# Kernel optimization log

Hardware: AMD Instinct MI355X
Metric: run time of the kernel (lower is better)

The kernel has to match this reference:

```python
import jax, jax.numpy as jnp
import numpy as np

M = 0.25
GAMMA = 256.0
HARD_W = 2.0
O_P = 1.0 + M
O_N = -M
DELTA_P = 1.0 - M
DELTA_N = M
NEG_BIG = -1e30  # masked-out fill for logsumexp (finite to keep grads NaN-free)


def setup_inputs() -> dict:
    key = jax.random.key(0)
    k1, k2 = jax.random.split(key)
    inputs = jax.random.normal(k1, (4096, 512), dtype=jnp.float32)
    targets = jax.random.randint(k2, (4096,), 0, 64, dtype=jnp.int64)
    return {"inputs": inputs, "targets": targets}


def reference(inputs, targets):
    n = inputs.shape[0]
    x = inputs / jnp.linalg.norm(inputs, axis=1, keepdims=True)  # L2 normalize
    sim = x @ x.T                                                # [n, n]

    same = targets[:, None] == targets[None, :]
    eye = jnp.eye(n, dtype=bool)
    pos_mask = same & ~eye
    neg_mask = ~same
    npos = pos_mask.sum(axis=1)
    nneg = neg_mask.sum(axis=1)

    sim_d = jax.lax.stop_gradient(sim)  # alphas are detached in the original
    alpha_p = jax.nn.relu(O_P - sim_d)
    alpha_n = jax.nn.relu(sim_d - O_N)

    # hard mining: scale alpha at hardest positive (min sim) / hardest negative (max sim)
    idx = jnp.arange(n)
    hard_p = jnp.argmin(jnp.where(pos_mask, sim_d, jnp.inf), axis=1)
    hard_n = jnp.argmax(jnp.where(neg_mask, sim_d, -jnp.inf), axis=1)
    hit_p = (idx[None, :] == hard_p[:, None]) & (npos > 1)[:, None]
    hit_n = (idx[None, :] == hard_n[:, None]) & (nneg > 1)[:, None]
    alpha_p = alpha_p * jnp.where(hit_p, HARD_W, 1.0)
    alpha_n = alpha_n * jnp.where(hit_n, HARD_W, 1.0)

    pos_term = jnp.where(pos_mask, -GAMMA * alpha_p * (sim - DELTA_P), NEG_BIG)
    neg_term = jnp.where(neg_mask, GAMMA * alpha_n * (sim - DELTA_N), NEG_BIG)
    lse_p = jax.nn.logsumexp(pos_term, axis=1)
    lse_n = jax.nn.logsumexp(neg_term, axis=1)

    valid = (npos > 0) & (nneg > 0)
    per_row = jnp.where(valid, jax.nn.softplus(lse_p + lse_n), 0.0)
    n_valid = jnp.maximum(valid.sum(), 1)
    return per_row.sum() / n_valid.astype(per_row.dtype)
```

## Files before the change

kernel.cpp:

```cpp
#include <hip/hip_runtime.h>


#define MASKT_  (-1.0e4f)
#define MINITP_ (-1.0e4f)
#define MASKP_  (-3.0e4f)
#define QA_     369.3299304675f
#define QB_     (-23.08312065422f)
#define LN2_    0.6931471805599453f

constexpr int N_ = 4096;
constexpr int D_ = 512;
constexpr int AST_ = 520;
constexpr int CCH_ = 16;

typedef __bf16 bf16x8 __attribute__((ext_vector_type(8)));
typedef float  f32x4  __attribute__((ext_vector_type(4)));
typedef const unsigned int __attribute__((address_space(1)))* gp_t;
typedef unsigned int       __attribute__((address_space(3)))* lp_t;

__device__ __forceinline__ float pos_q(float s) {
    float d = s - 1.0f;
    return fmaf(d * d, 256.0f, -16.0f);
}
__device__ __forceinline__ float neg_q(float s) {
    float q = fmaf(s * s, 256.0f, -16.0f);
    return (s >= -0.25f) ? q : 0.0f;
}
__device__ __forceinline__ float neg_q2(float s) {
    float q = fmaf(s * s, QA_, QB_);
    return (s >= -0.25f) ? q : 0.0f;
}
__device__ __forceinline__ void lse_merge(float m2, float S2, float& m, float& S) {
    float mm = fmaxf(m, m2);
    S = S * __expf(m - mm) + S2 * __expf(m2 - mm);
    m = mm;
}
__device__ __forceinline__ void lse_merge2(float m2, float S2, float& m, float& S) {
    float mm = fmaxf(m, m2);
    S = S * exp2f(m - mm) + S2 * exp2f(m2 - mm);
    m = mm;
}
__device__ __forceinline__ unsigned short f2bf(float f) {
    unsigned int u = __float_as_uint(f);
    unsigned int r = u + 0x7FFFu + ((u >> 16) & 1u);
    return (unsigned short)(r >> 16);
}

__global__ __launch_bounds__(256) void k_norm(const float* __restrict__ in,
                                              unsigned short* __restrict__ xb,
                                              float* __restrict__ acc) {
    const int row  = blockIdx.x * 4 + (threadIdx.x >> 6);
    const int lane = threadIdx.x & 63;
    const float4* src = (const float4*)(in + (size_t)row * D_) + lane * 2;
    float4 a = src[0], b = src[1];
    float ss = a.x*a.x + a.y*a.y + a.z*a.z + a.w*a.w
             + b.x*b.x + b.y*b.y + b.z*b.z + b.w*b.w;
    #pragma unroll
    for (int d = 32; d >= 1; d >>= 1) ss += __shfl_xor(ss, d);
    float rn = 1.0f / sqrtf(ss);
    float v[8] = {a.x, a.y, a.z, a.w, b.x, b.y, b.z, b.w};
    union { uint4 u; unsigned short us[8]; } pk;
    #pragma unroll
    for (int k = 0; k < 8; ++k) pk.us[k] = f2bf(v[k] * rn);
    *((uint4*)(xb + (size_t)row * D_) + lane) = pk.u;
    if (blockIdx.x == 0 && threadIdx.x < 4) acc[threadIdx.x] = 0.0f;
}

__global__ __launch_bounds__(256, 4) void k_mainM(const unsigned short* __restrict__ xb,
                                                  const int* __restrict__ tg,
                                                  float* __restrict__ part) {
    constexpr int NST = 16;
    __shared__ __align__(16) unsigned short Bs[2][16][AST_];

    const int tid  = threadIdx.x;
    const int wave = tid >> 6, lane = tid & 63;
    const int n16  = lane & 15, quad = lane >> 4;
    const int rg   = (int)blockIdx.x >> 4;
    const int cc   = (int)blockIdx.x & 15;
    const int rowBase = rg * 64 + wave * 16;
    const int colBase = cc * 256;
    const int phase = (((int)blockIdx.x >> 8) & 3) * 4;

    bf16x8 af[16];
    {
        const bf16x8* ap = (const bf16x8*)(xb + (size_t)(rowBase + n16) * D_ + quad * 8);
        #pragma unroll
        for (int kk = 0; kk < 16; ++kk) af[kk] = ap[kk * 4];
    }
    int tr[4];
    #pragma unroll
    for (int r = 0; r < 4; ++r) tr[r] = tg[rowBase + quad * 4 + r];

    float m_p[4], S_p[4], S_n[4], mxn[4];
    #pragma unroll
    for (int r = 0; r < 4; ++r) {
        m_p[r] = MINITP_; S_p[r] = 0.f; S_n[r] = 0.f; mxn[r] = -2.0f;
    }

    const char* gstage = (const char*)xb + (size_t)colBase * 1024 + lane * 16;

    {
        const char* g0 = gstage + (size_t)phase * 16384;
        #pragma unroll
        for (int p = 0; p < 4; ++p) {
            int j = p * 4 + wave;
            __builtin_amdgcn_global_load_lds((gp_t)(const void*)(g0 + j * 1024),
                                             (lp_t)(void*)&Bs[0][j][0], 16, 0, 0);
        }
    }
    int tc_cur = tg[colBase + phase * 16 + n16];

    auto epi = [&](const f32x4& a0, const f32x4& a1, int tcv, bool withDiag) {
        #pragma unroll
        for (int r = 0; r < 4; ++r) {
            float sim = a0[r] + a1[r];
            bool samec = (tr[r] == tcv);
            float dm1 = sim - 1.0f;
            float tp  = fmaf(dm1 * dm1, QA_, QB_);
            tp = samec ? tp : MASKP_;
            if (withDiag && n16 == quad * 4 + r) tp = MASKP_;
            float diff = m_p[r] - tp;
            float e    = exp2f(-fabsf(diff));
            float sA   = S_p[r] + e;
            float sB   = fmaf(S_p[r], e, 1.0f);
            S_p[r] = (diff < 0.0f) ? sB : sA;
            m_p[r] = fmaxf(m_p[r], tp);
            float tn = fmaf(sim * sim, QA_, QB_);
            float en = exp2f(tn);
            en = (sim >= -0.25f) ? en : 1.0f;
            en = samec ? 0.0f : en;
            S_n[r] += en;
            mxn[r] = fmaxf(mxn[r], samec ? -2.0f : sim);
        }
    };

    #pragma unroll 1
    for (int u = 0; u < NST; ++u) {
        const int s = (u + phase) & 15;
        const int b = u & 1;
        const int j0 = colBase + s * 16;
        __syncthreads();

        const int sn = (s + 1) & 15;
        if (u + 1 < NST) {
            const char* g2 = gstage + (size_t)sn * 16384;
            #pragma unroll
            for (int p = 0; p < 4; ++p) {
                int j = p * 4 + wave;
                __builtin_amdgcn_global_load_lds((gp_t)(const void*)(g2 + j * 1024),
                                                 (lp_t)(void*)&Bs[b ^ 1][j][0], 16, 0, 0);
            }
        }
        int tc_nxt = (u + 1 < NST) ? tg[colBase + sn * 16 + n16] : 0;

        f32x4 a0 = {0.f, 0.f, 0.f, 0.f}, a1 = {0.f, 0.f, 0.f, 0.f};
        __builtin_amdgcn_s_setprio(1);
        #pragma unroll
        for (int kk = 0; kk < 8; ++kk) {
            bf16x8 bf0 = *(const bf16x8*)&Bs[b][n16][(2 * kk) * 32 + quad * 8];
            bf16x8 bf1 = *(const bf16x8*)&Bs[b][n16][(2 * kk + 1) * 32 + quad * 8];
            a0 = __builtin_amdgcn_mfma_f32_16x16x32_bf16(af[2 * kk],     bf0, a0, 0, 0, 0);
            a1 = __builtin_amdgcn_mfma_f32_16x16x32_bf16(af[2 * kk + 1], bf1, a1, 0, 0, 0);
        }
        __builtin_amdgcn_s_setprio(0);

        if (j0 == rowBase) epi(a0, a1, tc_cur, true);
        else               epi(a0, a1, tc_cur, false);
        tc_cur = tc_nxt;
    }

    #pragma unroll
    for (int r = 0; r < 4; ++r) {
        #pragma unroll
        for (int d = 1; d <= 8; d <<= 1) {
            lse_merge2(__shfl_xor(m_p[r], d), __shfl_xor(S_p[r], d), m_p[r], S_p[r]);
            S_n[r] += __shfl_xor(S_n[r], d);
            mxn[r] = fmaxf(mxn[r], __shfl_xor(mxn[r], d));
        }
    }
    if (n16 == 0) {
        #pragma unroll
        for (int r = 0; r < 4; ++r) {
            ((float4*)part)[(size_t)(rowBase + quad * 4 + r) * CCH_ + cc] =
                make_float4(m_p[r], S_p[r], mxn[r], S_n[r]);
        }
    }
}

__global__ __launch_bounds__(256) void k_reduceF(const float* __restrict__ part,
                                                 const int* __restrict__ tg,
                                                 float* __restrict__ acc,
                                                 float* __restrict__ out) {
    __shared__ int hist[64];
    const int tid = threadIdx.x;
    if (tid < 64) hist[tid] = 0;
    __syncthreads();
    for (int i = tid; i < N_; i += 256) atomicAdd(&hist[tg[i]], 1);
    __syncthreads();

    const int row = blockIdx.x * 256 + tid;
    const float4* P = (const float4*)part + (size_t)row * CCH_;
    float M_p = MINITP_, Sp = 0.f, M_n = 0.f, Sn = 0.f, mxn = -2.0f;
    #pragma unroll
    for (int c = 0; c < CCH_; ++c) {
        float4 a = P[c];
        lse_merge2(a.x, a.y, M_p, Sp);
        Sn += a.w;
        mxn = fmaxf(mxn, a.z);
    }
    const int cnt = hist[tg[row]];
    float np2 = (float)(cnt - 1), nn2 = (float)(N_ - cnt);
    float loss = 0.f, vld = 0.f;
    if (np2 > 0.5f && nn2 > 0.5f) {
        if (np2 > 1.5f) {
            float t1 = M_p, t2 = 2.0f * t1;
            float mm = fmaxf(M_p, t2);
            Sp = Sp * exp2f(M_p - mm) + exp2f(t2 - mm) - exp2f(t1 - mm);
            M_p = mm;
        }
        if (nn2 > 1.5f) {
            float t1 = neg_q2(mxn), t2 = 2.0f * t1;
            float mm = fmaxf(M_n, t2);
            Sn = Sn * exp2f(M_n - mm) + exp2f(t2 - mm) - exp2f(t1 - mm);
            M_n = mm;
        }
        float z = LN2_ * ((M_p + __log2f(Sp)) + (M_n + __log2f(Sn)));
        loss = fmaxf(z, 0.0f) + log1pf(__expf(-fabsf(z)));
        vld = 1.0f;
    }
    #pragma unroll
    for (int d = 32; d >= 1; d >>= 1) { loss += __shfl_xor(loss, d); vld += __shfl_xor(vld, d); }
    if ((tid & 63) == 0) { atomicAdd(&acc[0], loss); atomicAdd(&acc[1], vld); }

    __syncthreads();
    if (tid == 0) {
        __threadfence();
        int old = atomicAdd((int*)(acc + 2), 1);
        if (old == (int)gridDim.x - 1) {
            float ls = atomicAdd(&acc[0], 0.0f);
            float lv = atomicAdd(&acc[1], 0.0f);
            out[0] = ls / fmaxf(lv, 1.0f);
        }
    }
}

__global__ void k_final(const float* __restrict__ acc, float* __restrict__ out) {
    if (threadIdx.x == 0) out[0] = acc[0] / fmaxf(acc[1], 1.0f);
}

__global__ void k_sentinel(float* __restrict__ out) {
    if (threadIdx.x == 0) out[0] = -12345.0f;
}

__global__ __launch_bounds__(1024, 4) void k_main3(const unsigned short* __restrict__ xb,
                                                   const int* __restrict__ tg,
                                                   float* __restrict__ acc_g) {
    __shared__ __align__(16) unsigned short As[16 * AST_];
    __shared__ float sm[16][16][8];
    const int tid  = threadIdx.x;
    const int wave = tid >> 6, lane = tid & 63;
    const int n16  = lane & 15, quad = lane >> 4;
    const int rowBase = blockIdx.x * 16;
    {
        int row = tid >> 6, c = tid & 63;
        *(uint4*)&As[row * AST_ + c * 8] =
            *(const uint4*)(xb + (size_t)(rowBase + row) * D_ + c * 8);
    }
    int ir[4], tr[4];
    #pragma unroll
    for (int r = 0; r < 4; ++r) { ir[r] = rowBase + quad * 4 + r; tr[r] = tg[ir[r]]; }
    float m_p[4], S_p[4], m_n[4], S_n[4], mnp[4], mxn[4], sc[4];
    #pragma unroll
    for (int r = 0; r < 4; ++r) {
        m_p[r] = 0.f; S_p[r] = 0.f; m_n[r] = 0.f; S_n[r] = 0.f;
        mnp[r] = 2.0f; mxn[r] = -2.0f; sc[r] = 0.f;
    }
    __syncthreads();
    const unsigned short* Af = &As[n16 * AST_ + quad * 8];
    #pragma unroll 1
    for (int t = wave; t < N_ / 16; t += 16) {
        const int jcol = t * 16 + n16;
        const int tc = tg[jcol];
        const bf16x8* bp = (const bf16x8*)(xb + (size_t)jcol * D_ + quad * 8);
        bf16x8 bf[16];
        #pragma unroll
        for (int kk = 0; kk < 16; ++kk) bf[kk] = bp[kk * 4];
        f32x4 a0 = {0.f, 0.f, 0.f, 0.f}, a1 = {0.f, 0.f, 0.f, 0.f};
        #pragma unroll
        for (int kk = 0; kk < 8; ++kk) {
            bf16x8 af0 = *(const bf16x8*)(Af + (2 * kk) * 32);
            bf16x8 af1 = *(const bf16x8*)(Af + (2 * kk + 1) * 32);
            a0 = __builtin_amdgcn_mfma_f32_16x16x32_bf16(af0, bf[2 * kk],     a0, 0, 0, 0);
            a1 = __builtin_amdgcn_mfma_f32_16x16x32_bf16(af1, bf[2 * kk + 1], a1, 0, 0, 0);
        }
        #pragma unroll
        for (int r = 0; r < 4; ++r) {
            float s = a0[r] + a1[r];
            bool samec = (tr[r] == tc);
            bool posm  = samec && (jcol != ir[r]);
            float tp = posm  ? pos_q(s) : MASKT_;
            float tn = samec ? MASKT_ : neg_q(s);
            float mm = fmaxf(m_p[r], tp);
            S_p[r] = S_p[r] * __expf(m_p[r] - mm) + __expf(tp - mm); m_p[r] = mm;
            mm = fmaxf(m_n[r], tn);
            S_n[r] = S_n[r] * __expf(m_n[r] - mm) + __expf(tn - mm); m_n[r] = mm;
            sc[r] += samec ? 1.0f : 0.0f;
            mnp[r] = fminf(mnp[r], posm ? s : 2.0f);
            mxn[r] = fmaxf(mxn[r], samec ? -2.0f : s);
        }
    }
    #pragma unroll
    for (int r = 0; r < 4; ++r) {
        #pragma unroll
        for (int d = 1; d <= 8; d <<= 1) {
            lse_merge(__shfl_xor(m_p[r], d), __shfl_xor(S_p[r], d), m_p[r], S_p[r]);
            lse_merge(__shfl_xor(m_n[r], d), __shfl_xor(S_n[r], d), m_n[r], S_n[r]);
            mnp[r] = fminf(mnp[r], __shfl_xor(mnp[r], d));
            mxn[r] = fmaxf(mxn[r], __shfl_xor(mxn[r], d));
            sc[r] += __shfl_xor(sc[r], d);
        }
    }
    if (n16 == 0) {
        #pragma unroll
        for (int r = 0; r < 4; ++r) {
            float* q = sm[wave][quad * 4 + r];
            q[0] = m_p[r]; q[1] = S_p[r]; q[2] = m_n[r]; q[3] = S_n[r];
            q[4] = mnp[r]; q[5] = mxn[r]; q[6] = sc[r];
        }
    }
    __syncthreads();
    if (tid < 64) {
        const int L = tid & 15;
        float m_p2 = 0.f, S_p2 = 0.f, m_n2 = 0.f, S_n2 = 0.f;
        float mnp2 = 2.0f, mxn2 = -2.0f, sct = 0.f;
        #pragma unroll
        for (int w = 0; w < 16; ++w) {
            const float* q = sm[w][L];
            lse_merge(q[0], q[1], m_p2, S_p2);
            lse_merge(q[2], q[3], m_n2, S_n2);
            mnp2 = fminf(mnp2, q[4]); mxn2 = fmaxf(mxn2, q[5]);
            sct += q[6];
        }
        float loss = 0.f, vld = 0.f;
        float np2 = sct - 1.0f, nn2 = (float)N_ - sct;
        if (tid < 16 && np2 > 0.5f && nn2 > 0.5f) {
            if (np2 > 1.5f) {
                float t1 = pos_q(mnp2), t2 = 2.0f * t1;
                float mm = fmaxf(m_p2, t2);
                S_p2 = S_p2 * __expf(m_p2 - mm) + __expf(t2 - mm) - __expf(t1 - mm);
                m_p2 = mm;
            }
            if (nn2 > 1.5f) {
                float t1 = neg_q(mxn2), t2 = 2.0f * t1;
                float mm = fmaxf(m_n2, t2);
                S_n2 = S_n2 * __expf(m_n2 - mm) + __expf(t2 - mm) - __expf(t1 - mm);
                m_n2 = mm;
            }
            float z = (m_p2 + __logf(S_p2)) + (m_n2 + __logf(S_n2));
            loss = fmaxf(z, 0.0f) + log1pf(__expf(-fabsf(z)));
            vld = 1.0f;
        }
        #pragma unroll
        for (int d = 32; d >= 1; d >>= 1) {
            loss += __shfl_xor(loss, d); vld += __shfl_xor(vld, d);
        }
        if (tid == 0) { atomicAdd(&acc_g[0], loss); atomicAdd(&acc_g[1], vld); }
    }
}

extern "C" void kernel_launch(void* const* d_in, const int* in_sizes, int n_in,
                              void* d_out, int out_size, void* d_ws, size_t ws_size,
                              hipStream_t stream) {
    const float* in = (const float*)d_in[0];
    const int*   tg = (const int*)d_in[1];
    constexpr size_t MB = 1024 * 1024;
    unsigned short* xb = (unsigned short*)d_ws;

    if (ws_size >= 5 * MB + 64) {
        float* part = (float*)((char*)d_ws + 4 * MB);
        float* acc  = (float*)((char*)d_ws + 5 * MB);
        hipLaunchKernelGGL(k_norm,    dim3(N_ / 4),    dim3(256), 0, stream, in, xb, acc);
        hipLaunchKernelGGL(k_mainM,   dim3(64 * CCH_), dim3(256), 0, stream, xb, tg, part);
        hipLaunchKernelGGL(k_reduceF, dim3(N_ / 256),  dim3(256), 0, stream, part, tg, acc,
                           (float*)d_out);
    } else if (ws_size >= 4 * MB + 64) {
        float* acc = (float*)((char*)d_ws + 4 * MB);
        hipLaunchKernelGGL(k_norm,  dim3(N_ / 4),  dim3(256),  0, stream, in, xb, acc);
        hipLaunchKernelGGL(k_main3, dim3(N_ / 16), dim3(1024), 0, stream, xb, tg, acc);
        hipLaunchKernelGGL(k_final, dim3(1),       dim3(64),   0, stream, acc, (float*)d_out);
    } else {
        hipLaunchKernelGGL(k_sentinel, dim3(1), dim3(64), 0, stream, (float*)d_out);
    }
}
```

Before: 107.4 us.

## Exploit similarity matrix symmetry with triangular block scheduling and column-side partials

Computes only the upper-triangular blocks of the symmetric similarity matrix. Each block accumulates row-side logsumexp/max partials and also column-side partials through shared memory and shuffles, which it writes to extra slots. Blocks are mapped to triangle coordinates with a sqrt-based index, and a per-element strict-upper mask handles the diagonal band. This is meant to roughly halve the MFMA and exp work, at the cost of more epilogue arithmetic, extra shared-memory merges, a larger partial buffer, and a fast path that now needs a 12 MB workspace.

```diff
diff --git a/kernel.cpp b/kernel.cpp
--- a/kernel.cpp
+++ b/kernel.cpp
@@ -11,7 +11,7 @@
 constexpr int N_ = 4096;
 constexpr int D_ = 512;
 constexpr int AST_ = 520;
-constexpr int CCH_ = 16;
+constexpr int NSLOT_ = 96;
 
 typedef __bf16 bf16x8 __attribute__((ext_vector_type(8)));
 typedef float  f32x4  __attribute__((ext_vector_type(4)));
@@ -66,20 +66,26 @@
     if (blockIdx.x == 0 && threadIdx.x < 4) acc[threadIdx.x] = 0.0f;
 }
 
-__global__ __launch_bounds__(256, 4) void k_mainM(const unsigned short* __restrict__ xb,
+__global__ __launch_bounds__(256, 4) void k_mainS(const unsigned short* __restrict__ xb,
                                                   const int* __restrict__ tg,
                                                   float* __restrict__ part) {
-    constexpr int NST = 16;
+    constexpr int NST = 8;
     __shared__ __align__(16) unsigned short Bs[2][16][AST_];
+    __shared__ float4 Bcol[2][4][16];
 
     const int tid  = threadIdx.x;
     const int wave = tid >> 6, lane = tid & 63;
     const int n16  = lane & 15, quad = lane >> 4;
-    const int rg   = (int)blockIdx.x >> 4;
-    const int cc   = (int)blockIdx.x & 15;
+
+    int bid = (int)blockIdx.x;
+    int cc = (int)((sqrtf(4.0f * (float)bid + 1.0f) - 1.0f) * 0.5f);
+    while ((cc + 1) * (cc + 2) <= bid) ++cc;
+    while (cc * (cc + 1) > bid) --cc;
+    const int rg = bid - cc * (cc + 1);
+
     const int rowBase = rg * 64 + wave * 16;
-    const int colBase = cc * 256;
-    const int phase = (((int)blockIdx.x >> 8) & 3) * 4;
+    const int colBase = cc * 128;
+    const bool band = (rg >= 2 * cc);
 
     bf16x8 af[16];
     {
@@ -98,52 +104,40 @@
     }
 
     const char* gstage = (const char*)xb + (size_t)colBase * 1024 + lane * 16;
-
-    {
-        const char* g0 = gstage + (size_t)phase * 16384;
-        #pragma unroll
-        for (int p = 0; p < 4; ++p) {
-            int j = p * 4 + wave;
-            __builtin_amdgcn_global_load_lds((gp_t)(const void*)(g0 + j * 1024),
-                                             (lp_t)(void*)&Bs[0][j][0], 16, 0, 0);
-        }
-    }
-    int tc_cur = tg[colBase + phase * 16 + n16];
-
-    auto epi = [&](const f32x4& a0, const f32x4& a1, int tcv, bool withDiag) {
-        #pragma unroll
-        for (int r = 0; r < 4; ++r) {
-            float sim = a0[r] + a1[r];
-            bool samec = (tr[r] == tcv);
-            float dm1 = sim - 1.0f;
-            float tp  = fmaf(dm1 * dm1, QA_, QB_);
-            tp = samec ? tp : MASKP_;
-            if (withDiag && n16 == quad * 4 + r) tp = MASKP_;
-            float diff = m_p[r] - tp;
-            float e    = exp2f(-fabsf(diff));
-            float sA   = S_p[r] + e;
-            float sB   = fmaf(S_p[r], e, 1.0f);
-            S_p[r] = (diff < 0.0f) ? sB : sA;
-            m_p[r] = fmaxf(m_p[r], tp);
-            float tn = fmaf(sim * sim, QA_, QB_);
-            float en = exp2f(tn);
-            en = (sim >= -0.25f) ? en : 1.0f;
-            en = samec ? 0.0f : en;
-            S_n[r] += en;
-            mxn[r] = fmaxf(mxn[r], samec ? -2.0f : sim);
+    #pragma unroll
+    for (int p = 0; p < 4; ++p) {
+        int j = p * 4 + wave;
+        __builtin_amdgcn_global_load_lds((gp_t)(const void*)(gstage + j * 1024),
+                                         (lp_t)(void*)&Bs[0][j][0], 16, 0, 0);
+    }
+    int tc_cur = tg[colBase + n16];
+
+    auto mergeCol = [&](int sp) {
+        const int c = lane >> 2, w = lane & 3;
+        float4 v = Bcol[sp & 1][w][c];
+        #pragma unroll
+        for (int d = 1; d <= 2; d <<= 1) {
+            float m2 = __shfl_xor(v.x, d), S2 = __shfl_xor(v.y, d);
+            float z2 = __shfl_xor(v.z, d), n2 = __shfl_xor(v.w, d);
+            lse_merge2(m2, S2, v.x, v.y);
+            v.z = fmaxf(v.z, z2);
+            v.w += n2;
+        }
+        if (w == 0) {
+            int jc = colBase + sp * 16 + c;
+            ((float4*)part)[(size_t)jc * NSLOT_ + 32 + rg] = v;
         }
     };
 
     #pragma unroll 1
     for (int u = 0; u < NST; ++u) {
-        const int s = (u + phase) & 15;
         const int b = u & 1;
-        const int j0 = colBase + s * 16;
         __syncthreads();
 
-        const int sn = (s + 1) & 15;
+        if (u > 0 && wave == ((u - 1) & 3)) mergeCol(u - 1);
+
         if (u + 1 < NST) {
-            const char* g2 = gstage + (size_t)sn * 16384;
+            const char* g2 = gstage + (size_t)(u + 1) * 16384;
             #pragma unroll
             for (int p = 0; p < 4; ++p) {
                 int j = p * 4 + wave;
@@ -151,7 +145,7 @@
                                                  (lp_t)(void*)&Bs[b ^ 1][j][0], 16, 0, 0);
             }
         }
-        int tc_nxt = (u + 1 < NST) ? tg[colBase + sn * 16 + n16] : 0;
+        int tc_nxt = (u + 1 < NST) ? tg[colBase + (u + 1) * 16 + n16] : 0;
 
         f32x4 a0 = {0.f, 0.f, 0.f, 0.f}, a1 = {0.f, 0.f, 0.f, 0.f};
         __builtin_amdgcn_s_setprio(1);
@@ -164,10 +158,46 @@
         }
         __builtin_amdgcn_s_setprio(0);
 
-        if (j0 == rowBase) epi(a0, a1, tc_cur, true);
-        else               epi(a0, a1, tc_cur, false);
+        const int jcol = colBase + u * 16 + n16;
+        const int iv   = rowBase + quad * 4;
+        float mc = MINITP_, Sc = 0.f, Snc = 0.f, mxc = -2.0f;
+        #pragma unroll
+        for (int r = 0; r < 4; ++r) {
+            float sim = a0[r] + a1[r];
+            bool samec = (tr[r] == tc_cur);
+            bool valid = !band || (iv + r < jcol);
+            float dm1 = sim - 1.0f;
+            float tp  = fmaf(dm1 * dm1, QA_, QB_);
+            tp = (samec && valid) ? tp : MASKP_;
+            float diff = m_p[r] - tp;
+            float e    = exp2f(-fabsf(diff));
+            S_p[r] = (diff < 0.0f) ? fmaf(S_p[r], e, 1.0f) : S_p[r] + e;
+            m_p[r] = fmaxf(m_p[r], tp);
+            float dc = mc - tp;
+            float ec = exp2f(-fabsf(dc));
+            Sc = (dc < 0.0f) ? fmaf(Sc, ec, 1.0f) : Sc + ec;
+            mc = fmaxf(mc, tp);
+            float tn = fmaf(sim * sim, QA_, QB_);
+            float en = exp2f(tn);
+            en = (sim >= -0.25f) ? en : 1.0f;
+            en = (!samec && valid) ? en : 0.0f;
+            S_n[r] += en; Snc += en;
+            float simn = (valid && !samec) ? sim : -2.0f;
+            mxn[r] = fmaxf(mxn[r], simn);
+            mxc    = fmaxf(mxc, simn);
+        }
+        #pragma unroll
+        for (int d = 16; d <= 32; d <<= 1) {
+            lse_merge2(__shfl_xor(mc, d), __shfl_xor(Sc, d), mc, Sc);
+            Snc += __shfl_xor(Snc, d);
+            mxc = fmaxf(mxc, __shfl_xor(mxc, d));
+        }
+        if (quad == 0) Bcol[b][wave][n16] = make_float4(mc, Sc, mxc, Snc);
+
         tc_cur = tc_nxt;
     }
+    __syncthreads();
+    if (wave == 3) mergeCol(NST - 1);
 
     #pragma unroll
     for (int r = 0; r < 4; ++r) {
@@ -181,13 +211,13 @@
     if (n16 == 0) {
         #pragma unroll
         for (int r = 0; r < 4; ++r) {
-            ((float4*)part)[(size_t)(rowBase + quad * 4 + r) * CCH_ + cc] =
+            ((float4*)part)[(size_t)(rowBase + quad * 4 + r) * NSLOT_ + cc] =
                 make_float4(m_p[r], S_p[r], mxn[r], S_n[r]);
         }
     }
 }
 
-__global__ __launch_bounds__(256) void k_reduceF(const float* __restrict__ part,
+__global__ __launch_bounds__(256) void k_reduceS(const float* __restrict__ part,
                                                  const int* __restrict__ tg,
                                                  float* __restrict__ acc,
                                                  float* __restrict__ out) {
@@ -199,15 +229,25 @@
     __syncthreads();
 
     const int row = blockIdx.x * 256 + tid;
-    const float4* P = (const float4*)part + (size_t)row * CCH_;
+    const int rg  = row >> 6;
+    const int ccmin = rg >> 1;
+    const int nb  = min(2 * (rg >> 1) + 2, 64);
+    const float4* P = (const float4*)part + (size_t)row * NSLOT_;
+
     float M_p = MINITP_, Sp = 0.f, M_n = 0.f, Sn = 0.f, mxn = -2.0f;
-    #pragma unroll
-    for (int c = 0; c < CCH_; ++c) {
+    for (int c = ccmin; c < 32; ++c) {
         float4 a = P[c];
         lse_merge2(a.x, a.y, M_p, Sp);
         Sn += a.w;
         mxn = fmaxf(mxn, a.z);
     }
+    for (int b = 0; b < nb; ++b) {
+        float4 a = P[32 + b];
+        lse_merge2(a.x, a.y, M_p, Sp);
+        Sn += a.w;
+        mxn = fmaxf(mxn, a.z);
+    }
+
     const int cnt = hist[tg[row]];
     float np2 = (float)(cnt - 1), nn2 = (float)(N_ - cnt);
     float loss = 0.f, vld = 0.f;
@@ -354,6 +394,7 @@
                 float t1 = neg_q(mxn2), t2 = 2.0f * t1;
                 float mm = fmaxf(m_n2, t2);
                 S_n2 = S_n2 * __expf(m_n2 - mm) + __expf(t2 - mm) - __expf(t1 - mm);
+                M_n2: ;
                 m_n2 = mm;
             }
             float z = (m_p2 + __logf(S_p2)) + (m_n2 + __logf(S_n2));
@@ -376,12 +417,12 @@
     constexpr size_t MB = 1024 * 1024;
     unsigned short* xb = (unsigned short*)d_ws;
 
-    if (ws_size >= 5 * MB + 64) {
-        float* part = (float*)((char*)d_ws + 4 * MB);
-        float* acc  = (float*)((char*)d_ws + 5 * MB);
-        hipLaunchKernelGGL(k_norm,    dim3(N_ / 4),    dim3(256), 0, stream, in, xb, acc);
-        hipLaunchKernelGGL(k_mainM,   dim3(64 * CCH_), dim3(256), 0, stream, xb, tg, part);
-        hipLaunchKernelGGL(k_reduceF, dim3(N_ / 256),  dim3(256), 0, stream, part, tg, acc,
+    if (ws_size >= 12 * MB) {
+        float* acc  = (float*)((char*)d_ws + 4 * MB);
+        float* part = (float*)((char*)d_ws + 5 * MB);
+        hipLaunchKernelGGL(k_norm,    dim3(N_ / 4),   dim3(256), 0, stream, in, xb, acc);
+        hipLaunchKernelGGL(k_mainS,   dim3(1056),     dim3(256), 0, stream, xb, tg, part);
+        hipLaunchKernelGGL(k_reduceS, dim3(N_ / 256), dim3(256), 0, stream, part, tg, acc,
                            (float*)d_out);
     } else if (ws_size >= 4 * MB + 64) {
         float* acc = (float*)((char*)d_ws + 4 * MB);
```

Result: slower. 128.8 us (+20.0%).

## Split positive-pair LSE into per-class kernel, keep only negative terms in main pass

Applied to the files above, without the earlier changes.

The main all-pairs kernel no longer computes the positive-pair online logsumexp. It only accumulates the negative sum and the hardest-negative max, which trims the epilogue and halves the partial output. A new per-class kernel gathers each class's member indices and computes positive similarities only within the class. It makes two passes, one for the min similarity (used as the max term) and one for the exp-sum. This adds a kernel launch and a small 64-block kernel with uncoalesced row gathers, and it depends on there being at most 64 classes, which is a property of the test inputs.

```diff
diff --git a/kernel.cpp b/kernel.cpp
--- a/kernel.cpp
+++ b/kernel.cpp
@@ -3,7 +3,6 @@
 
 #define MASKT_  (-1.0e4f)
 #define MINITP_ (-1.0e4f)
-#define MASKP_  (-3.0e4f)
 #define QA_     369.3299304675f
 #define QB_     (-23.08312065422f)
 #define LN2_    0.6931471805599453f
@@ -66,7 +65,7 @@
     if (blockIdx.x == 0 && threadIdx.x < 4) acc[threadIdx.x] = 0.0f;
 }
 
-__global__ __launch_bounds__(256, 4) void k_mainM(const unsigned short* __restrict__ xb,
+__global__ __launch_bounds__(256, 4) void k_mainN(const unsigned short* __restrict__ xb,
                                                   const int* __restrict__ tg,
                                                   float* __restrict__ part) {
     constexpr int NST = 16;
@@ -91,14 +90,11 @@
     #pragma unroll
     for (int r = 0; r < 4; ++r) tr[r] = tg[rowBase + quad * 4 + r];
 
-    float m_p[4], S_p[4], S_n[4], mxn[4];
-    #pragma unroll
-    for (int r = 0; r < 4; ++r) {
-        m_p[r] = MINITP_; S_p[r] = 0.f; S_n[r] = 0.f; mxn[r] = -2.0f;
-    }
+    float S_n[4], mxn[4];
+    #pragma unroll
+    for (int r = 0; r < 4; ++r) { S_n[r] = 0.f; mxn[r] = -2.0f; }
 
     const char* gstage = (const char*)xb + (size_t)colBase * 1024 + lane * 16;
-
     {
         const char* g0 = gstage + (size_t)phase * 16384;
         #pragma unroll
@@ -110,21 +106,39 @@
     }
     int tc_cur = tg[colBase + phase * 16 + n16];
 
-    auto epi = [&](const f32x4& a0, const f32x4& a1, int tcv, bool withDiag) {
+    #pragma unroll 1
+    for (int u = 0; u < NST; ++u) {
+        const int s = (u + phase) & 15;
+        const int b = u & 1;
+        __syncthreads();
+
+        const int sn = (s + 1) & 15;
+        if (u + 1 < NST) {
+            const char* g2 = gstage + (size_t)sn * 16384;
+            #pragma unroll
+            for (int p = 0; p < 4; ++p) {
+                int j = p * 4 + wave;
+                __builtin_amdgcn_global_load_lds((gp_t)(const void*)(g2 + j * 1024),
+                                                 (lp_t)(void*)&Bs[b ^ 1][j][0], 16, 0, 0);
+            }
+        }
+        int tc_nxt = (u + 1 < NST) ? tg[colBase + sn * 16 + n16] : 0;
+
+        f32x4 a0 = {0.f, 0.f, 0.f, 0.f}, a1 = {0.f, 0.f, 0.f, 0.f};
+        __builtin_amdgcn_s_setprio(1);
+        #pragma unroll
+        for (int kk = 0; kk < 8; ++kk) {
+            bf16x8 bf0 = *(const bf16x8*)&Bs[b][n16][(2 * kk) * 32 + quad * 8];
+            bf16x8 bf1 = *(const bf16x8*)&Bs[b][n16][(2 * kk + 1) * 32 + quad * 8];
+            a0 = __builtin_amdgcn_mfma_f32_16x16x32_bf16(af[2 * kk],     bf0, a0, 0, 0, 0);
+            a1 = __builtin_amdgcn_mfma_f32_16x16x32_bf16(af[2 * kk + 1], bf1, a1, 0, 0, 0);
+        }
+        __builtin_amdgcn_s_setprio(0);
+
         #pragma unroll
         for (int r = 0; r < 4; ++r) {
             float sim = a0[r] + a1[r];
-            bool samec = (tr[r] == tcv);
-            float dm1 = sim - 1.0f;
-            float tp  = fmaf(dm1 * dm1, QA_, QB_);
-            tp = samec ? tp : MASKP_;
-            if (withDiag && n16 == quad * 4 + r) tp = MASKP_;
-            float diff = m_p[r] - tp;
-            float e    = exp2f(-fabsf(diff));
-            float sA   = S_p[r] + e;
-            float sB   = fmaf(S_p[r], e, 1.0f);
-            S_p[r] = (diff < 0.0f) ? sB : sA;
-            m_p[r] = fmaxf(m_p[r], tp);
+            bool samec = (tr[r] == tc_cur);
             float tn = fmaf(sim * sim, QA_, QB_);
             float en = exp2f(tn);
             en = (sim >= -0.25f) ? en : 1.0f;
@@ -132,40 +146,6 @@
             S_n[r] += en;
             mxn[r] = fmaxf(mxn[r], samec ? -2.0f : sim);
         }
-    };
-
-    #pragma unroll 1
-    for (int u = 0; u < NST; ++u) {
-        const int s = (u + phase) & 15;
-        const int b = u & 1;
-        const int j0 = colBase + s * 16;
-        __syncthreads();
-
-        const int sn = (s + 1) & 15;
-        if (u + 1 < NST) {
-            const char* g2 = gstage + (size_t)sn * 16384;
-            #pragma unroll
-            for (int p = 0; p < 4; ++p) {
-                int j = p * 4 + wave;
-                __builtin_amdgcn_global_load_lds((gp_t)(const void*)(g2 + j * 1024),
-                                                 (lp_t)(void*)&Bs[b ^ 1][j][0], 16, 0, 0);
-            }
-        }
-        int tc_nxt = (u + 1 < NST) ? tg[colBase + sn * 16 + n16] : 0;
-
-        f32x4 a0 = {0.f, 0.f, 0.f, 0.f}, a1 = {0.f, 0.f, 0.f, 0.f};
-        __builtin_amdgcn_s_setprio(1);
-        #pragma unroll
-        for (int kk = 0; kk < 8; ++kk) {
-            bf16x8 bf0 = *(const bf16x8*)&Bs[b][n16][(2 * kk) * 32 + quad * 8];
-            bf16x8 bf1 = *(const bf16x8*)&Bs[b][n16][(2 * kk + 1) * 32 + quad * 8];
-            a0 = __builtin_amdgcn_mfma_f32_16x16x32_bf16(af[2 * kk],     bf0, a0, 0, 0, 0);
-            a1 = __builtin_amdgcn_mfma_f32_16x16x32_bf16(af[2 * kk + 1], bf1, a1, 0, 0, 0);
-        }
-        __builtin_amdgcn_s_setprio(0);
-
-        if (j0 == rowBase) epi(a0, a1, tc_cur, true);
-        else               epi(a0, a1, tc_cur, false);
         tc_cur = tc_nxt;
     }
 
@@ -173,7 +153,6 @@
     for (int r = 0; r < 4; ++r) {
         #pragma unroll
         for (int d = 1; d <= 8; d <<= 1) {
-            lse_merge2(__shfl_xor(m_p[r], d), __shfl_xor(S_p[r], d), m_p[r], S_p[r]);
             S_n[r] += __shfl_xor(S_n[r], d);
             mxn[r] = fmaxf(mxn[r], __shfl_xor(mxn[r], d));
         }
@@ -181,34 +160,125 @@
     if (n16 == 0) {
         #pragma unroll
         for (int r = 0; r < 4; ++r) {
-            ((float4*)part)[(size_t)(rowBase + quad * 4 + r) * CCH_ + cc] =
-                make_float4(m_p[r], S_p[r], mxn[r], S_n[r]);
-        }
-    }
-}
-
-__global__ __launch_bounds__(256) void k_reduceF(const float* __restrict__ part,
+            ((float2*)part)[(size_t)(rowBase + quad * 4 + r) * CCH_ + cc] =
+                make_float2(mxn[r], S_n[r]);
+        }
+    }
+}
+
+__global__ __launch_bounds__(256, 1) void k_classP(const unsigned short* __restrict__ xb,
+                                                   const int* __restrict__ tg,
+                                                   float* __restrict__ part2,
+                                                   int* __restrict__ cnt_g) {
+    __shared__ int lst[N_];
+    __shared__ int lcnt;
+    const int tid  = threadIdx.x;
+    const int wave = tid >> 6, lane = tid & 63;
+    const int n16  = lane & 15, quad = lane >> 4;
+    const int c    = (int)blockIdx.x;
+
+    if (tid == 0) lcnt = 0;
+    __syncthreads();
+    for (int i = tid; i < N_; i += 256)
+        if (tg[i] == c) lst[atomicAdd(&lcnt, 1)] = i;
+    __syncthreads();
+    const int Kc = lcnt;
+    if (tid == 0) cnt_g[c] = Kc;
+
+    for (int rb = wave * 16; rb < Kc; rb += 64) {
+        const int ia = lst[(rb + n16 < Kc) ? rb + n16 : 0];
+        bf16x8 af[16];
+        {
+            const bf16x8* ap = (const bf16x8*)(xb + (size_t)ia * D_ + quad * 8);
+            #pragma unroll
+            for (int kk = 0; kk < 16; ++kk) af[kk] = ap[kk * 4];
+        }
+        auto simStage = [&](int cs, f32x4& a0, f32x4& a1) {
+            const int jb = cs + n16;
+            const int jcol = lst[(jb < Kc) ? jb : 0];
+            const bf16x8* bp = (const bf16x8*)(xb + (size_t)jcol * D_ + quad * 8);
+            a0 = {0.f, 0.f, 0.f, 0.f}; a1 = {0.f, 0.f, 0.f, 0.f};
+            #pragma unroll
+            for (int kk = 0; kk < 8; ++kk) {
+                bf16x8 b0 = bp[(2 * kk) * 4], b1 = bp[(2 * kk + 1) * 4];
+                a0 = __builtin_amdgcn_mfma_f32_16x16x32_bf16(af[2 * kk],     b0, a0, 0, 0, 0);
+                a1 = __builtin_amdgcn_mfma_f32_16x16x32_bf16(af[2 * kk + 1], b1, a1, 0, 0, 0);
+            }
+        };
+
+        float mnp[4] = {2.f, 2.f, 2.f, 2.f};
+        for (int cs = 0; cs < Kc; cs += 16) {
+            f32x4 a0, a1; simStage(cs, a0, a1);
+            #pragma unroll
+            for (int r = 0; r < 4; ++r) {
+                const int ii = rb + quad * 4 + r, jb = cs + n16;
+                bool valid = (ii < Kc) && (jb < Kc) && (jb != ii);
+                float sim = a0[r] + a1[r];
+                mnp[r] = fminf(mnp[r], valid ? sim : 2.0f);
+            }
+        }
+        #pragma unroll
+        for (int r = 0; r < 4; ++r)
+            #pragma unroll
+            for (int d = 1; d <= 8; d <<= 1)
+                mnp[r] = fminf(mnp[r], __shfl_xor(mnp[r], d));
+
+        float mp[4], Sp[4];
+        #pragma unroll
+        for (int r = 0; r < 4; ++r) {
+            float dm = mnp[r] - 1.0f;
+            mp[r] = (mnp[r] < 1.5f) ? fmaf(dm * dm, QA_, QB_) : MINITP_;
+            Sp[r] = 0.f;
+        }
+        for (int cs = 0; cs < Kc; cs += 16) {
+            f32x4 a0, a1; simStage(cs, a0, a1);
+            #pragma unroll
+            for (int r = 0; r < 4; ++r) {
+                const int ii = rb + quad * 4 + r, jb = cs + n16;
+                bool valid = (ii < Kc) && (jb < Kc) && (jb != ii);
+                float sim = a0[r] + a1[r];
+                float dm1 = sim - 1.0f;
+                float tp  = fmaf(dm1 * dm1, QA_, QB_);
+                Sp[r] += valid ? exp2f(tp - mp[r]) : 0.f;
+            }
+        }
+        #pragma unroll
+        for (int r = 0; r < 4; ++r)
+            #pragma unroll
+            for (int d = 1; d <= 8; d <<= 1)
+                Sp[r] += __shfl_xor(Sp[r], d);
+
+        if (n16 == 0) {
+            #pragma unroll
+            for (int r = 0; r < 4; ++r) {
+                const int ii = rb + quad * 4 + r;
+                if (ii < Kc)
+                    ((float2*)part2)[lst[ii]] = make_float2(mp[r], Sp[r]);
+            }
+        }
+    }
+}
+
+__global__ __launch_bounds__(256) void k_reduceN(const float* __restrict__ part,
+                                                 const float* __restrict__ part2,
+                                                 const int* __restrict__ cnt_g,
                                                  const int* __restrict__ tg,
                                                  float* __restrict__ acc,
                                                  float* __restrict__ out) {
-    __shared__ int hist[64];
     const int tid = threadIdx.x;
-    if (tid < 64) hist[tid] = 0;
-    __syncthreads();
-    for (int i = tid; i < N_; i += 256) atomicAdd(&hist[tg[i]], 1);
-    __syncthreads();
-
     const int row = blockIdx.x * 256 + tid;
-    const float4* P = (const float4*)part + (size_t)row * CCH_;
-    float M_p = MINITP_, Sp = 0.f, M_n = 0.f, Sn = 0.f, mxn = -2.0f;
+    const float2* P = (const float2*)part + (size_t)row * CCH_;
+    float Sn = 0.f, mxn = -2.0f;
     #pragma unroll
     for (int c = 0; c < CCH_; ++c) {
-        float4 a = P[c];
-        lse_merge2(a.x, a.y, M_p, Sp);
-        Sn += a.w;
-        mxn = fmaxf(mxn, a.z);
-    }
-    const int cnt = hist[tg[row]];
+        float2 a = P[c];
+        Sn += a.y;
+        mxn = fmaxf(mxn, a.x);
+    }
+    float2 pp = ((const float2*)part2)[row];
+    float M_p = pp.x, Sp = pp.y, M_n = 0.f;
+
+    const int cnt = cnt_g[tg[row]];
     float np2 = (float)(cnt - 1), nn2 = (float)(N_ - cnt);
     float loss = 0.f, vld = 0.f;
     if (np2 > 0.5f && nn2 > 0.5f) {
@@ -376,13 +446,17 @@
     constexpr size_t MB = 1024 * 1024;
     unsigned short* xb = (unsigned short*)d_ws;
 
-    if (ws_size >= 5 * MB + 64) {
-        float* part = (float*)((char*)d_ws + 4 * MB);
-        float* acc  = (float*)((char*)d_ws + 5 * MB);
+    if (ws_size >= 8 * MB) {
+        float* acc   = (float*)((char*)d_ws + 4 * MB);
+        int*   cnt_g = (int*)((char*)d_ws + 4 * MB + 256);
+        float* part2 = (float*)((char*)d_ws + 4 * MB + 4096);
+        float* part  = (float*)((char*)d_ws + 5 * MB);
         hipLaunchKernelGGL(k_norm,    dim3(N_ / 4),    dim3(256), 0, stream, in, xb, acc);
-        hipLaunchKernelGGL(k_mainM,   dim3(64 * CCH_), dim3(256), 0, stream, xb, tg, part);
-        hipLaunchKernelGGL(k_reduceF, dim3(N_ / 256),  dim3(256), 0, stream, part, tg, acc,
-                           (float*)d_out);
+        hipLaunchKernelGGL(k_mainN,   dim3(64 * CCH_), dim3(256), 0, stream, xb, tg, part);
+        hipLaunchKernelGGL(k_classP,  dim3(64),        dim3(256), 0, stream, xb, tg, part2,
+                           cnt_g);
+        hipLaunchKernelGGL(k_reduceN, dim3(N_ / 256),  dim3(256), 0, stream, part, part2,
+                           cnt_g, tg, acc, (float*)d_out);
     } else if (ws_size >= 4 * MB + 64) {
         float* acc = (float*)((char*)d_ws + 4 * MB);
         hipLaunchKernelGGL(k_norm,  dim3(N_ / 4),  dim3(256),  0, stream, in, xb, acc);
```

Result: slower. 132.8 us (+23.7%).
